# Performance work log

Hardware: AMD Instinct MI355X
Metric: run time of the kernel (lower is better)

Reference implementation:

```python
import jax, jax.numpy as jnp
import numpy as np

N_NODES = 50000
N_EDGES = 200000
IN_DIM = 512
HID = 2000
LAT = 128


def setup_inputs() -> dict:
    key = jax.random.key(0)
    ks = jax.random.split(key, 6)
    x = jax.random.normal(ks[0], (N_NODES, IN_DIM), dtype=jnp.float32)
    edge_index = jax.random.randint(ks[1], (2, N_EDGES), 0, N_NODES, dtype=jnp.int64)
    # glorot-ish scales so ReLU/Sigmoid stay in a sane range
    W1 = jax.random.normal(ks[2], (IN_DIM, HID), dtype=jnp.float32) * (1.0 / np.sqrt(IN_DIM))
    b1 = jnp.zeros((HID,), dtype=jnp.float32)
    W2 = jax.random.normal(ks[3], (HID, LAT), dtype=jnp.float32) * (1.0 / np.sqrt(HID))
    b2 = jnp.zeros((LAT,), dtype=jnp.float32)
    return {"x": x, "edge_index": edge_index, "W1": W1, "b1": b1, "W2": W2, "b2": b2}


def gcn_conv(x, edge_index, W, b):
    """PyG GCNConv: D^-1/2 (A+I) D^-1/2 (X W) + b, unit edge weights."""
    n = x.shape[0]
    loops = jnp.arange(n, dtype=edge_index.dtype)
    row = jnp.concatenate([edge_index[0], loops])  # source nodes
    col = jnp.concatenate([edge_index[1], loops])  # target nodes
    deg = jax.ops.segment_sum(jnp.ones_like(col, dtype=x.dtype), col, num_segments=n)
    dis = jnp.where(deg > 0, jax.lax.rsqrt(deg), 0.0)  # deg^-1/2, inf -> 0
    norm = dis[row] * dis[col]                         # [E+N]
    h = x @ W                                          # transform first: [N, out]
    msg = h[row] * norm[:, None]                       # gather + normalize: [E+N, out]
    out = jax.ops.segment_sum(msg, col, num_segments=n)  # scatter-add
    return out + b


def reference(x, edge_index, W1, b1, W2, b2):
    h = jax.nn.relu(gcn_conv(x, edge_index, W1, b1))
    return jax.nn.sigmoid(gcn_conv(h, edge_index, W2, b2))
```

## Files before the change

### kernel.cpp

```cpp
#include <hip/hip_runtime.h>
#include <hip/hip_fp16.h>

#define NN 50000
#define NE 200000
#define IND 512
#define HIDD 2000
#define LATD 128

#define M_PAD 50176
#define N1_PAD 2048
#define MT1 392
#define NBLK 196

typedef _Float16 f16x8 __attribute__((ext_vector_type(8)));
typedef float f32x4 __attribute__((ext_vector_type(4)));

__device__ __forceinline__ void gload_lds16(const _Float16* g, _Float16* l) {
    __builtin_amdgcn_global_load_lds(
        (const __attribute__((address_space(1))) unsigned int*)g,
        (__attribute__((address_space(3))) unsigned int*)l,
        16, 0, 0);
}

__global__ void k_degree(const int* __restrict__ col, int* __restrict__ deg) {
    int e = blockIdx.x * 256 + threadIdx.x;
    if (e < NE) atomicAdd(&deg[col[e]], 1);
}

__global__ void k_bsum(const int* __restrict__ deg, int* __restrict__ bsum) {
    __shared__ int sm[4];
    int i = blockIdx.x * 256 + threadIdx.x;
    int v = (i < NN) ? deg[i] : 0;
    #pragma unroll
    for (int off = 32; off; off >>= 1) v += __shfl_down(v, off, 64);
    if ((threadIdx.x & 63) == 0) sm[threadIdx.x >> 6] = v;
    __syncthreads();
    if (threadIdx.x == 0) bsum[blockIdx.x] = sm[0] + sm[1] + sm[2] + sm[3];
}

__global__ void k_bscan(int* __restrict__ bsum) {
    __shared__ int sm[256];
    int tid = threadIdx.x;
    int v = (tid < NBLK) ? bsum[tid] : 0;
    sm[tid] = v;
    __syncthreads();
    #pragma unroll
    for (int off = 1; off < 256; off <<= 1) {
        int t = (tid >= off) ? sm[tid - off] : 0;
        __syncthreads();
        sm[tid] += t;
        __syncthreads();
    }
    if (tid < NBLK) bsum[tid] = sm[tid] - v;
}

__global__ void k_scan_final(const int* __restrict__ deg, const int* __restrict__ bsum,
                             int* __restrict__ row_ptr, float* __restrict__ dis) {
    __shared__ int sm[256];
    int b = blockIdx.x, tid = threadIdx.x;
    int i = b * 256 + tid;
    int v = (i < NN) ? deg[i] : 0;
    if (i < NN) dis[i] = rsqrtf((float)v + 1.0f);
    sm[tid] = v;
    __syncthreads();
    #pragma unroll
    for (int off = 1; off < 256; off <<= 1) {
        int t = (tid >= off) ? sm[tid - off] : 0;
        __syncthreads();
        sm[tid] += t;
        __syncthreads();
    }
    if (i < NN) row_ptr[i] = bsum[b] + sm[tid] - v;
    if (i == NN - 1) row_ptr[NN] = bsum[b] + sm[tid];
}

__global__ void k_fill(const int* __restrict__ ei, const int* __restrict__ row_ptr,
                       int* __restrict__ cursor, int* __restrict__ csr_src) {
    int e = blockIdx.x * 256 + threadIdx.x;
    if (e < NE) {
        int r = ei[e], c = ei[NE + e];
        int pos = atomicAdd(&cursor[c], 1);
        csr_src[row_ptr[c] + pos] = r;
    }
}

__global__ void k_transpose_tiled(const float* __restrict__ in,
                                  _Float16* __restrict__ out, int R, int C, int ldo,
                                  int Rpad, int Cpad) {
    __shared__ float sm[32][33];
    int c0 = blockIdx.x * 32, r0 = blockIdx.y * 32;
    int tx = threadIdx.x & 31, ty = threadIdx.x >> 5;
    #pragma unroll
    for (int i = 0; i < 4; ++i) {
        int r = r0 + ty + i * 8, c = c0 + tx;
        sm[ty + i * 8][tx] = (r < R && c < C) ? in[(size_t)r * C + c] : 0.f;
    }
    __syncthreads();
    #pragma unroll
    for (int i = 0; i < 4; ++i) {
        int c = c0 + ty + i * 8, r = r0 + tx;
        if (c < Cpad && r < Rpad) out[(size_t)c * ldo + r] = (_Float16)sm[tx][ty + i * 8];
    }
}

__global__ void k_xcvt(const float* __restrict__ in, _Float16* __restrict__ out, int n8) {
    int i = blockIdx.x * 256 + threadIdx.x;
    if (i < n8) {
        float4 a = ((const float4*)in)[i * 2];
        float4 b = ((const float4*)in)[i * 2 + 1];
        f16x8 o;
        o[0] = (_Float16)a.x; o[1] = (_Float16)a.y; o[2] = (_Float16)a.z; o[3] = (_Float16)a.w;
        o[4] = (_Float16)b.x; o[5] = (_Float16)b.y; o[6] = (_Float16)b.z; o[7] = (_Float16)b.w;
        ((f16x8*)out)[i] = o;
    }
}

__global__ void k_gather_x(const _Float16* __restrict__ xh, const int* __restrict__ row_ptr,
                           const int* __restrict__ csr_src, const float* __restrict__ dis,
                           _Float16* __restrict__ Ah) {
    int dst = blockIdx.x * 4 + (threadIdx.x >> 6);
    if (dst >= NN) return;
    int lane = threadIdx.x & 63;
    float dd = dis[dst];
    const f16x8* vb = (const f16x8*)xh;
    f16x8 sv = vb[(size_t)dst * 64 + lane];
    float acc[8];
    #pragma unroll
    for (int q = 0; q < 8; ++q) acc[q] = dd * (float)sv[q];
    int beg = row_ptr[dst], end = row_ptr[dst + 1];
    for (int c = beg; c < end; c += 64) {
        int n = end - c; if (n > 64) n = 64;
        int li = (lane < n) ? csr_src[c + lane] : 0;
        float lns = (lane < n) ? dis[li] : 0.f;
        for (int j = 0; j < n; j += 4) {
            int j1 = j + 1 < n ? j + 1 : n - 1;
            int j2 = j + 2 < n ? j + 2 : n - 1;
            int j3 = j + 3 < n ? j + 3 : n - 1;
            int s0 = __shfl(li, j),  s1 = __shfl(li, j1);
            int s2 = __shfl(li, j2), s3 = __shfl(li, j3);
            float w0 = __shfl(lns, j);
            float w1 = (j + 1 < n) ? __shfl(lns, j1) : 0.f;
            float w2 = (j + 2 < n) ? __shfl(lns, j2) : 0.f;
            float w3 = (j + 3 < n) ? __shfl(lns, j3) : 0.f;
            f16x8 v0 = vb[(size_t)s0 * 64 + lane];
            f16x8 v1 = vb[(size_t)s1 * 64 + lane];
            f16x8 v2 = vb[(size_t)s2 * 64 + lane];
            f16x8 v3 = vb[(size_t)s3 * 64 + lane];
            #pragma unroll
            for (int q = 0; q < 8; ++q)
                acc[q] += w0 * (float)v0[q] + w1 * (float)v1[q]
                        + w2 * (float)v2[q] + w3 * (float)v3[q];
        }
    }
    f16x8 o;
    #pragma unroll
    for (int q = 0; q < 8; ++q) o[q] = (_Float16)(dd * acc[q]);
    *(f16x8*)(Ah + (size_t)dst * IND + lane * 8) = o;
}

__global__ void k_gather_t(const float* __restrict__ t, const int* __restrict__ row_ptr,
                           const int* __restrict__ csr_src, const float* __restrict__ dis,
                           const float* __restrict__ b2, float* __restrict__ out) {
    int dst = blockIdx.x * 4 + (threadIdx.x >> 6);
    if (dst >= NN) return;
    int lane = threadIdx.x & 63;
    float dd = dis[dst];
    const float2* vb = (const float2*)t;
    float2 td = vb[(size_t)dst * 64 + lane];
    float accx = dd * td.x, accy = dd * td.y;
    int beg = row_ptr[dst], end = row_ptr[dst + 1];
    for (int c = beg; c < end; c += 64) {
        int n = end - c; if (n > 64) n = 64;
        int li = (lane < n) ? csr_src[c + lane] : 0;
        float lns = (lane < n) ? dis[li] : 0.f;
        for (int j = 0; j < n; j += 4) {
            int j1 = j + 1 < n ? j + 1 : n - 1;
            int j2 = j + 2 < n ? j + 2 : n - 1;
            int j3 = j + 3 < n ? j + 3 : n - 1;
            int s0 = __shfl(li, j),  s1 = __shfl(li, j1);
            int s2 = __shfl(li, j2), s3 = __shfl(li, j3);
            float w0 = __shfl(lns, j);
            float w1 = (j + 1 < n) ? __shfl(lns, j1) : 0.f;
            float w2 = (j + 2 < n) ? __shfl(lns, j2) : 0.f;
            float w3 = (j + 3 < n) ? __shfl(lns, j3) : 0.f;
            float2 v0 = vb[(size_t)s0 * 64 + lane];
            float2 v1 = vb[(size_t)s1 * 64 + lane];
            float2 v2 = vb[(size_t)s2 * 64 + lane];
            float2 v3 = vb[(size_t)s3 * 64 + lane];
            accx += w0 * v0.x + w1 * v1.x + w2 * v2.x + w3 * v3.x;
            accy += w0 * v0.y + w1 * v1.y + w2 * v2.y + w3 * v3.y;
        }
    }
    float2 bb = *(const float2*)(b2 + lane * 2);
    float vx = dd * accx + bb.x;
    float vy = dd * accy + bb.y;
    float2 o;
    o.x = 1.0f / (1.0f + __expf(-vx));
    o.y = 1.0f / (1.0f + __expf(-vy));
    *(float2*)(out + (size_t)dst * LATD + lane * 2) = o;
}

__global__ __launch_bounds__(256, 2) void k_gemm1(
    const _Float16* __restrict__ A,
    const _Float16* __restrict__ Bt,
    const float* __restrict__ bias,
    _Float16* __restrict__ Ch,
    int mT0, int slab)
{
    const int b = blockIdx.x;
    const int mT = mT0 + (b & 7) * slab + ((b >> 3) >> 4);
    const int nT = (b >> 3) & 15;
    const int mBase = mT * 128;
    const int nBase = nT * 128;

    __shared__ __align__(16) _Float16 As[2 * 128 * 32];
    __shared__ __align__(16) _Float16 Bs[2 * 128 * 32];

    const int tid = threadIdx.x;
    const int lane = tid & 63;
    const int w = tid >> 6;

    const int srow = w * 32 + (lane >> 2);
    const int scol = (lane & 3) * 8;
    const _Float16* Ag0 = A + (size_t)(mBase + srow) * IND + scol;
    const _Float16* Ag1 = Ag0 + (size_t)16 * IND;
    const _Float16* Bg0 = Bt + (size_t)(nBase + srow) * IND + scol;
    const _Float16* Bg1 = Bg0 + (size_t)16 * IND;

    const int wm = (w >> 1) * 64;
    const int wn = (w & 1) * 64;
    const int lm = lane & 15;
    const int quad = lane >> 4;

    f32x4 acc[4][4];
    #pragma unroll
    for (int i = 0; i < 4; ++i)
        #pragma unroll
        for (int j = 0; j < 4; ++j)
            acc[i][j] = (f32x4){0.f, 0.f, 0.f, 0.f};

    for (int k0 = 0; k0 < IND; k0 += 64) {
        #pragma unroll
        for (int s = 0; s < 2; ++s) {
            gload_lds16(Ag0 + k0 + s * 32, As + s * 4096 + w * 1024);
            gload_lds16(Ag1 + k0 + s * 32, As + s * 4096 + w * 1024 + 512);
            gload_lds16(Bg0 + k0 + s * 32, Bs + s * 4096 + w * 1024);
            gload_lds16(Bg1 + k0 + s * 32, Bs + s * 4096 + w * 1024 + 512);
        }
        __syncthreads();

        #pragma unroll
        for (int s = 0; s < 2; ++s) {
            f16x8 af[4], bfr[4];
            #pragma unroll
            for (int mi = 0; mi < 4; ++mi)
                af[mi] = *(const f16x8*)&As[s * 4096 + (wm + mi * 16 + lm) * 32 + quad * 8];
            #pragma unroll
            for (int ni = 0; ni < 4; ++ni)
                bfr[ni] = *(const f16x8*)&Bs[s * 4096 + (wn + ni * 16 + lm) * 32 + quad * 8];
            #pragma unroll
            for (int mi = 0; mi < 4; ++mi)
                #pragma unroll
                for (int ni = 0; ni < 4; ++ni)
                    acc[mi][ni] = __builtin_amdgcn_mfma_f32_16x16x32_f16(
                        af[mi], bfr[ni], acc[mi][ni], 0, 0, 0);
        }
        __syncthreads();
    }

    #pragma unroll
    for (int mi = 0; mi < 4; ++mi) {
        #pragma unroll
        for (int ni = 0; ni < 4; ++ni) {
            int col = nBase + wn + ni * 16 + lm;
            float bval = (col < HIDD) ? bias[col] : 0.f;
            #pragma unroll
            for (int r = 0; r < 4; ++r) {
                int rowg = mBase + wm + mi * 16 + quad * 4 + r;
                float v = fmaxf(acc[mi][ni][r] + bval, 0.f);
                Ch[(size_t)rowg * N1_PAD + col] = (_Float16)v;
            }
        }
    }
}

__global__ __launch_bounds__(256, 2) void k_gemm2(
    const _Float16* __restrict__ A,
    const _Float16* __restrict__ Bt,
    float* __restrict__ Cf)
{
    __shared__ __align__(16) _Float16 As[2 * 4096];
    __shared__ __align__(16) _Float16 Bs[2 * 8192];

    const int tid = threadIdx.x;
    const int lane = tid & 63;
    const int w = tid >> 6;
    const int mBase = blockIdx.x * 64;

    const int srA = w * 16 + (lane >> 2);
    const int srB = w * 32 + (lane >> 2);
    const int scol = (lane & 3) * 8;
    const _Float16* Ag  = A + (size_t)(mBase + srA) * N1_PAD + scol;
    const _Float16* Bg0 = Bt + (size_t)srB * N1_PAD + scol;
    const _Float16* Bg1 = Bg0 + (size_t)16 * N1_PAD;

    const int wm = (w & 1) * 32;
    const int wn = (w >> 1) * 64;
    const int lm = lane & 15;
    const int quad = lane >> 4;

    f32x4 acc[2][4];
    #pragma unroll
    for (int i = 0; i < 2; ++i)
        #pragma unroll
        for (int j = 0; j < 4; ++j)
            acc[i][j] = (f32x4){0.f, 0.f, 0.f, 0.f};

    auto STAGE = [&](int buf, int k0) {
        #pragma unroll
        for (int s = 0; s < 2; ++s) {
            gload_lds16(Ag + k0 + s * 32, As + buf * 4096 + s * 2048 + w * 512);
            gload_lds16(Bg0 + k0 + s * 32, Bs + buf * 8192 + s * 4096 + w * 1024);
            gload_lds16(Bg1 + k0 + s * 32, Bs + buf * 8192 + s * 4096 + w * 1024 + 512);
        }
    };
    auto COMPUTE = [&](int buf) {
        #pragma unroll
        for (int s = 0; s < 2; ++s) {
            f16x8 af[2], bfr[4];
            #pragma unroll
            for (int mi = 0; mi < 2; ++mi)
                af[mi] = *(const f16x8*)&As[buf * 4096 + s * 2048 + (wm + mi * 16 + lm) * 32 + quad * 8];
            #pragma unroll
            for (int ni = 0; ni < 4; ++ni)
                bfr[ni] = *(const f16x8*)&Bs[buf * 8192 + s * 4096 + (wn + ni * 16 + lm) * 32 + quad * 8];
            #pragma unroll
            for (int mi = 0; mi < 2; ++mi)
                #pragma unroll
                for (int ni = 0; ni < 4; ++ni)
                    acc[mi][ni] = __builtin_amdgcn_mfma_f32_16x16x32_f16(
                        af[mi], bfr[ni], acc[mi][ni], 0, 0, 0);
        }
    };

    STAGE(0, 0);
    __syncthreads();
    #pragma unroll 1
    for (int it = 0; it < 15; ++it) {
        STAGE(1, (2 * it + 1) * 64);
        COMPUTE(0);
        __syncthreads();
        STAGE(0, (2 * it + 2) * 64);
        COMPUTE(1);
        __syncthreads();
    }
    STAGE(1, 31 * 64);
    COMPUTE(0);
    __syncthreads();
    COMPUTE(1);

    #pragma unroll
    for (int mi = 0; mi < 2; ++mi) {
        #pragma unroll
        for (int ni = 0; ni < 4; ++ni) {
            int col = wn + ni * 16 + lm;
            #pragma unroll
            for (int r = 0; r < 4; ++r) {
                int rowg = mBase + wm + mi * 16 + quad * 4 + r;
                Cf[(size_t)rowg * LATD + col] = acc[mi][ni][r];
            }
        }
    }
}

extern "C" void kernel_launch(void* const* d_in, const int* in_sizes, int n_in,
                              void* d_out, int out_size, void* d_ws, size_t ws_size,
                              hipStream_t stream) {
    const float* x  = (const float*)d_in[0];
    const int* ei   = (const int*)d_in[1];
    const float* W1 = (const float*)d_in[2];
    const float* b1 = (const float*)d_in[3];
    const float* W2 = (const float*)d_in[4];
    const float* b2 = (const float*)d_in[5];
    float* out = (float*)d_out;

    char* p = (char*)d_ws;
    auto alloc = [&](size_t bytes) {
        char* q = p; p += (bytes + 255) & ~(size_t)255; return q;
    };
    int* deg        = (int*)alloc((size_t)NN * 4);
    int* bsum       = (int*)alloc((size_t)NBLK * 4);
    int* row_ptr    = (int*)alloc((size_t)(NN + 1) * 4);
    int* cursor     = (int*)alloc((size_t)NN * 4);
    int* csr_src    = (int*)alloc((size_t)NE * 4);
    float* dis      = (float*)alloc((size_t)NN * 4);
    _Float16* W1T   = (_Float16*)alloc((size_t)N1_PAD * IND * 2);
    _Float16* W2T   = (_Float16*)alloc((size_t)LATD * N1_PAD * 2);
    _Float16* xh    = (_Float16*)alloc((size_t)NN * IND * 2);
    _Float16* Ah    = (_Float16*)alloc((size_t)M_PAD * IND * 2);
    _Float16* h     = (_Float16*)alloc((size_t)M_PAD * N1_PAD * 2);
    float* t        = (float*)alloc((size_t)M_PAD * LATD * 4);

    hipMemsetAsync(deg,    0, (size_t)NN * 4, stream);
    hipMemsetAsync(cursor, 0, (size_t)NN * 4, stream);

    k_degree<<<(NE + 255) / 256, 256, 0, stream>>>(ei + NE, deg);
    k_bsum<<<NBLK, 256, 0, stream>>>(deg, bsum);
    k_bscan<<<1, 256, 0, stream>>>(bsum);
    k_scan_final<<<NBLK, 256, 0, stream>>>(deg, bsum, row_ptr, dis);
    k_fill<<<(NE + 255) / 256, 256, 0, stream>>>(ei, row_ptr, cursor, csr_src);

    {
        dim3 gt1(N1_PAD / 32, IND / 32);
        k_transpose_tiled<<<gt1, 256, 0, stream>>>(W1, W1T, IND, HIDD, IND, IND, N1_PAD);
        dim3 gt2(LATD / 32, N1_PAD / 32);
        k_transpose_tiled<<<gt2, 256, 0, stream>>>(W2, W2T, HIDD, LATD, N1_PAD, N1_PAD, LATD);
        k_xcvt<<<(NN * IND / 8 + 255) / 256, 256, 0, stream>>>(x, xh, NN * IND / 8);
    }

    k_gather_x<<<(NN + 3) / 4, 256, 0, stream>>>(xh, row_ptr, csr_src, dis, Ah);

    k_gemm1<<<8 * 12 * 16, 256, 0, stream>>>(Ah, W1T, b1, h, 0,   12);
    k_gemm1<<<8 * 12 * 16, 256, 0, stream>>>(Ah, W1T, b1, h, 96,  12);
    k_gemm1<<<8 * 12 * 16, 256, 0, stream>>>(Ah, W1T, b1, h, 192, 12);
    k_gemm1<<<8 * 13 * 16, 256, 0, stream>>>(Ah, W1T, b1, h, 288, 13);
    k_gemm2<<<M_PAD / 64, 256, 0, stream>>>(h, W2T, t);

    k_gather_t<<<(NN + 3) / 4, 256, 0, stream>>>(t, row_ptr, csr_src, dis, b2, out);
}
```

Baseline: 502.4 us.

## Fuse both GEMMs into one kernel keeping hidden activations in LDS

Replaces the four GEMM1 launches and the separate GEMM2 with a single kernel. Each block computes 128-column chunks of the ReLU hidden layer for 64 rows, stores them in shared memory, and immediately multiplies them by the matching slice of W2. This removes the write and re-read of the 50176x2048 fp16 hidden matrix. In exchange, each block streams its A tile from global memory again for every chunk and reads W2 fragments directly from global. The GEMM1 tile shrinks to 64x128, and the loop is not double-buffered.

```diff
diff --git a/kernel.cpp b/kernel.cpp
--- a/kernel.cpp
+++ b/kernel.cpp
@@ -9,7 +9,6 @@
 
 #define M_PAD 50176
 #define N1_PAD 2048
-#define MT1 392
 #define NBLK 196
 
 typedef _Float16 f16x8 __attribute__((ext_vector_type(8)));
@@ -200,164 +199,112 @@
     *(float2*)(out + (size_t)dst * LATD + lane * 2) = o;
 }
 
-__global__ __launch_bounds__(256, 2) void k_gemm1(
+__global__ __launch_bounds__(256, 3) void k_fused(
     const _Float16* __restrict__ A,
-    const _Float16* __restrict__ Bt,
-    const float* __restrict__ bias,
-    _Float16* __restrict__ Ch,
-    int mT0, int slab)
-{
-    const int b = blockIdx.x;
-    const int mT = mT0 + (b & 7) * slab + ((b >> 3) >> 4);
-    const int nT = (b >> 3) & 15;
-    const int mBase = mT * 128;
-    const int nBase = nT * 128;
-
-    __shared__ __align__(16) _Float16 As[2 * 128 * 32];
-    __shared__ __align__(16) _Float16 Bs[2 * 128 * 32];
-
-    const int tid = threadIdx.x;
-    const int lane = tid & 63;
-    const int w = tid >> 6;
-
-    const int srow = w * 32 + (lane >> 2);
-    const int scol = (lane & 3) * 8;
-    const _Float16* Ag0 = A + (size_t)(mBase + srow) * IND + scol;
-    const _Float16* Ag1 = Ag0 + (size_t)16 * IND;
-    const _Float16* Bg0 = Bt + (size_t)(nBase + srow) * IND + scol;
-    const _Float16* Bg1 = Bg0 + (size_t)16 * IND;
-
-    const int wm = (w >> 1) * 64;
-    const int wn = (w & 1) * 64;
-    const int lm = lane & 15;
-    const int quad = lane >> 4;
-
-    f32x4 acc[4][4];
-    #pragma unroll
-    for (int i = 0; i < 4; ++i)
-        #pragma unroll
-        for (int j = 0; j < 4; ++j)
-            acc[i][j] = (f32x4){0.f, 0.f, 0.f, 0.f};
-
-    for (int k0 = 0; k0 < IND; k0 += 64) {
-        #pragma unroll
-        for (int s = 0; s < 2; ++s) {
-            gload_lds16(Ag0 + k0 + s * 32, As + s * 4096 + w * 1024);
-            gload_lds16(Ag1 + k0 + s * 32, As + s * 4096 + w * 1024 + 512);
-            gload_lds16(Bg0 + k0 + s * 32, Bs + s * 4096 + w * 1024);
-            gload_lds16(Bg1 + k0 + s * 32, Bs + s * 4096 + w * 1024 + 512);
-        }
-        __syncthreads();
-
-        #pragma unroll
-        for (int s = 0; s < 2; ++s) {
-            f16x8 af[4], bfr[4];
-            #pragma unroll
-            for (int mi = 0; mi < 4; ++mi)
-                af[mi] = *(const f16x8*)&As[s * 4096 + (wm + mi * 16 + lm) * 32 + quad * 8];
-            #pragma unroll
-            for (int ni = 0; ni < 4; ++ni)
-                bfr[ni] = *(const f16x8*)&Bs[s * 4096 + (wn + ni * 16 + lm) * 32 + quad * 8];
-            #pragma unroll
-            for (int mi = 0; mi < 4; ++mi)
-                #pragma unroll
-                for (int ni = 0; ni < 4; ++ni)
-                    acc[mi][ni] = __builtin_amdgcn_mfma_f32_16x16x32_f16(
-                        af[mi], bfr[ni], acc[mi][ni], 0, 0, 0);
-        }
-        __syncthreads();
-    }
-
-    #pragma unroll
-    for (int mi = 0; mi < 4; ++mi) {
-        #pragma unroll
-        for (int ni = 0; ni < 4; ++ni) {
-            int col = nBase + wn + ni * 16 + lm;
-            float bval = (col < HIDD) ? bias[col] : 0.f;
-            #pragma unroll
-            for (int r = 0; r < 4; ++r) {
-                int rowg = mBase + wm + mi * 16 + quad * 4 + r;
-                float v = fmaxf(acc[mi][ni][r] + bval, 0.f);
-                Ch[(size_t)rowg * N1_PAD + col] = (_Float16)v;
-            }
-        }
-    }
-}
-
-__global__ __launch_bounds__(256, 2) void k_gemm2(
-    const _Float16* __restrict__ A,
-    const _Float16* __restrict__ Bt,
+    const _Float16* __restrict__ B1,
+    const float* __restrict__ b1,
+    const _Float16* __restrict__ B2,
     float* __restrict__ Cf)
 {
-    __shared__ __align__(16) _Float16 As[2 * 4096];
-    __shared__ __align__(16) _Float16 Bs[2 * 8192];
+    __shared__ __align__(16) _Float16 As[2 * 64 * 32];
+    __shared__ __align__(16) _Float16 Bs[2 * 128 * 32];
+    __shared__ __align__(16) _Float16 hs[64 * 136];
 
     const int tid = threadIdx.x;
     const int lane = tid & 63;
     const int w = tid >> 6;
     const int mBase = blockIdx.x * 64;
 
-    const int srA = w * 16 + (lane >> 2);
-    const int srB = w * 32 + (lane >> 2);
+    const int srowA = w * 16 + (lane >> 2);
+    const int srowB = w * 32 + (lane >> 2);
     const int scol = (lane & 3) * 8;
-    const _Float16* Ag  = A + (size_t)(mBase + srA) * N1_PAD + scol;
-    const _Float16* Bg0 = Bt + (size_t)srB * N1_PAD + scol;
-    const _Float16* Bg1 = Bg0 + (size_t)16 * N1_PAD;
+    const _Float16* Ag = A + (size_t)(mBase + srowA) * IND + scol;
 
     const int wm = (w & 1) * 32;
     const int wn = (w >> 1) * 64;
     const int lm = lane & 15;
     const int quad = lane >> 4;
 
-    f32x4 acc[2][4];
+    f32x4 acc2[2][4];
     #pragma unroll
     for (int i = 0; i < 2; ++i)
         #pragma unroll
         for (int j = 0; j < 4; ++j)
-            acc[i][j] = (f32x4){0.f, 0.f, 0.f, 0.f};
-
-    auto STAGE = [&](int buf, int k0) {
-        #pragma unroll
-        for (int s = 0; s < 2; ++s) {
-            gload_lds16(Ag + k0 + s * 32, As + buf * 4096 + s * 2048 + w * 512);
-            gload_lds16(Bg0 + k0 + s * 32, Bs + buf * 8192 + s * 4096 + w * 1024);
-            gload_lds16(Bg1 + k0 + s * 32, Bs + buf * 8192 + s * 4096 + w * 1024 + 512);
-        }
-    };
-    auto COMPUTE = [&](int buf) {
-        #pragma unroll
-        for (int s = 0; s < 2; ++s) {
-            f16x8 af[2], bfr[4];
+            acc2[i][j] = (f32x4){0.f, 0.f, 0.f, 0.f};
+
+    #pragma unroll 1
+    for (int nc = 0; nc < 16; ++nc) {
+        f32x4 acc1[2][4];
+        #pragma unroll
+        for (int i = 0; i < 2; ++i)
+            #pragma unroll
+            for (int j = 0; j < 4; ++j)
+                acc1[i][j] = (f32x4){0.f, 0.f, 0.f, 0.f};
+
+        const _Float16* Bg0 = B1 + (size_t)(nc * 128 + srowB) * IND + scol;
+        const _Float16* Bg1 = Bg0 + (size_t)16 * IND;
+
+        for (int k0 = 0; k0 < IND; k0 += 64) {
+            #pragma unroll
+            for (int s = 0; s < 2; ++s) {
+                gload_lds16(Ag + k0 + s * 32, As + s * 2048 + w * 512);
+                gload_lds16(Bg0 + k0 + s * 32, Bs + s * 4096 + w * 1024);
+                gload_lds16(Bg1 + k0 + s * 32, Bs + s * 4096 + w * 1024 + 512);
+            }
+            __syncthreads();
+            #pragma unroll
+            for (int s = 0; s < 2; ++s) {
+                f16x8 af[2], bfr[4];
+                #pragma unroll
+                for (int mi = 0; mi < 2; ++mi)
+                    af[mi] = *(const f16x8*)&As[s * 2048 + (wm + mi * 16 + lm) * 32 + quad * 8];
+                #pragma unroll
+                for (int ni = 0; ni < 4; ++ni)
+                    bfr[ni] = *(const f16x8*)&Bs[s * 4096 + (wn + ni * 16 + lm) * 32 + quad * 8];
+                #pragma unroll
+                for (int mi = 0; mi < 2; ++mi)
+                    #pragma unroll
+                    for (int ni = 0; ni < 4; ++ni)
+                        acc1[mi][ni] = __builtin_amdgcn_mfma_f32_16x16x32_f16(
+                            af[mi], bfr[ni], acc1[mi][ni], 0, 0, 0);
+            }
+            __syncthreads();
+        }
+
+        #pragma unroll
+        for (int mi = 0; mi < 2; ++mi) {
+            #pragma unroll
+            for (int ni = 0; ni < 4; ++ni) {
+                int col = wn + ni * 16 + lm;
+                int gcol = nc * 128 + col;
+                float bval = (gcol < HIDD) ? b1[gcol] : 0.f;
+                #pragma unroll
+                for (int r = 0; r < 4; ++r) {
+                    int row = wm + mi * 16 + quad * 4 + r;
+                    hs[row * 136 + col] = (_Float16)fmaxf(acc1[mi][ni][r] + bval, 0.f);
+                }
+            }
+        }
+        __syncthreads();
+
+        #pragma unroll
+        for (int ks = 0; ks < 4; ++ks) {
+            f16x8 a2[2], b2f[4];
             #pragma unroll
             for (int mi = 0; mi < 2; ++mi)
-                af[mi] = *(const f16x8*)&As[buf * 4096 + s * 2048 + (wm + mi * 16 + lm) * 32 + quad * 8];
+                a2[mi] = *(const f16x8*)&hs[(wm + mi * 16 + lm) * 136 + ks * 32 + quad * 8];
             #pragma unroll
             for (int ni = 0; ni < 4; ++ni)
-                bfr[ni] = *(const f16x8*)&Bs[buf * 8192 + s * 4096 + (wn + ni * 16 + lm) * 32 + quad * 8];
+                b2f[ni] = *(const f16x8*)(B2 + (size_t)(wn + ni * 16 + lm) * N1_PAD
+                                          + nc * 128 + ks * 32 + quad * 8);
             #pragma unroll
             for (int mi = 0; mi < 2; ++mi)
                 #pragma unroll
                 for (int ni = 0; ni < 4; ++ni)
-                    acc[mi][ni] = __builtin_amdgcn_mfma_f32_16x16x32_f16(
-                        af[mi], bfr[ni], acc[mi][ni], 0, 0, 0);
-        }
-    };
-
-    STAGE(0, 0);
-    __syncthreads();
-    #pragma unroll 1
-    for (int it = 0; it < 15; ++it) {
-        STAGE(1, (2 * it + 1) * 64);
-        COMPUTE(0);
-        __syncthreads();
-        STAGE(0, (2 * it + 2) * 64);
-        COMPUTE(1);
-        __syncthreads();
-    }
-    STAGE(1, 31 * 64);
-    COMPUTE(0);
-    __syncthreads();
-    COMPUTE(1);
+                    acc2[mi][ni] = __builtin_amdgcn_mfma_f32_16x16x32_f16(
+                        a2[mi], b2f[ni], acc2[mi][ni], 0, 0, 0);
+        }
+    }
 
     #pragma unroll
     for (int mi = 0; mi < 2; ++mi) {
@@ -367,7 +314,7 @@
             #pragma unroll
             for (int r = 0; r < 4; ++r) {
                 int rowg = mBase + wm + mi * 16 + quad * 4 + r;
-                Cf[(size_t)rowg * LATD + col] = acc[mi][ni][r];
+                Cf[(size_t)rowg * LATD + col] = acc2[mi][ni][r];
             }
         }
     }
@@ -398,7 +345,6 @@
     _Float16* W2T   = (_Float16*)alloc((size_t)LATD * N1_PAD * 2);
     _Float16* xh    = (_Float16*)alloc((size_t)NN * IND * 2);
     _Float16* Ah    = (_Float16*)alloc((size_t)M_PAD * IND * 2);
-    _Float16* h     = (_Float16*)alloc((size_t)M_PAD * N1_PAD * 2);
     float* t        = (float*)alloc((size_t)M_PAD * LATD * 4);
 
     hipMemsetAsync(deg,    0, (size_t)NN * 4, stream);
@@ -420,11 +366,7 @@
 
     k_gather_x<<<(NN + 3) / 4, 256, 0, stream>>>(xh, row_ptr, csr_src, dis, Ah);
 
-    k_gemm1<<<8 * 12 * 16, 256, 0, stream>>>(Ah, W1T, b1, h, 0,   12);
-    k_gemm1<<<8 * 12 * 16, 256, 0, stream>>>(Ah, W1T, b1, h, 96,  12);
-    k_gemm1<<<8 * 12 * 16, 256, 0, stream>>>(Ah, W1T, b1, h, 192, 12);
-    k_gemm1<<<8 * 13 * 16, 256, 0, stream>>>(Ah, W1T, b1, h, 288, 13);
-    k_gemm2<<<M_PAD / 64, 256, 0, stream>>>(h, W2T, t);
+    k_fused<<<M_PAD / 64, 256, 0, stream>>>(Ah, W1T, b1, W2T, t);
 
     k_gather_t<<<(NN + 3) / 4, 256, 0, stream>>>(t, row_ptr, csr_src, dis, b2, out);
 }
```

Result: slower. 641.0 us (+27.6%).

## Enlarge gemm2 tile to 128 rows, store t in fp16, drop double buffering

Applied to the files above, without the earlier changes.

The second GEMM now works on 128x128 tiles with 4x4 MFMA fragments per wave, launched as 392 blocks in an interleaved order, and uses a single LDS buffer with a sync after loading instead of the previous double-buffered pipeline. The intermediate t is written and gathered in fp16 rather than fp32, halving the traffic of the final gather and of the GEMM output. The larger tile improves reuse of the loaded data, but dropping the overlap exposes load latency. The fp16 intermediate also loses a little precision.

```diff
diff --git a/kernel.cpp b/kernel.cpp
--- a/kernel.cpp
+++ b/kernel.cpp
@@ -9,10 +9,10 @@
 
 #define M_PAD 50176
 #define N1_PAD 2048
-#define MT1 392
 #define NBLK 196
 
 typedef _Float16 f16x8 __attribute__((ext_vector_type(8)));
+typedef _Float16 f16x2 __attribute__((ext_vector_type(2)));
 typedef float f32x4 __attribute__((ext_vector_type(4)));
 
 __device__ __forceinline__ void gload_lds16(const _Float16* g, _Float16* l) {
@@ -158,16 +158,16 @@
     *(f16x8*)(Ah + (size_t)dst * IND + lane * 8) = o;
 }
 
-__global__ void k_gather_t(const float* __restrict__ t, const int* __restrict__ row_ptr,
+__global__ void k_gather_t(const _Float16* __restrict__ t, const int* __restrict__ row_ptr,
                            const int* __restrict__ csr_src, const float* __restrict__ dis,
                            const float* __restrict__ b2, float* __restrict__ out) {
     int dst = blockIdx.x * 4 + (threadIdx.x >> 6);
     if (dst >= NN) return;
     int lane = threadIdx.x & 63;
     float dd = dis[dst];
-    const float2* vb = (const float2*)t;
-    float2 td = vb[(size_t)dst * 64 + lane];
-    float accx = dd * td.x, accy = dd * td.y;
+    const f16x2* vb = (const f16x2*)t;
+    f16x2 td = vb[(size_t)dst * 64 + lane];
+    float accx = dd * (float)td[0], accy = dd * (float)td[1];
     int beg = row_ptr[dst], end = row_ptr[dst + 1];
     for (int c = beg; c < end; c += 64) {
         int n = end - c; if (n > 64) n = 64;
@@ -183,12 +183,14 @@
             float w1 = (j + 1 < n) ? __shfl(lns, j1) : 0.f;
             float w2 = (j + 2 < n) ? __shfl(lns, j2) : 0.f;
             float w3 = (j + 3 < n) ? __shfl(lns, j3) : 0.f;
-            float2 v0 = vb[(size_t)s0 * 64 + lane];
-            float2 v1 = vb[(size_t)s1 * 64 + lane];
-            float2 v2 = vb[(size_t)s2 * 64 + lane];
-            float2 v3 = vb[(size_t)s3 * 64 + lane];
-            accx += w0 * v0.x + w1 * v1.x + w2 * v2.x + w3 * v3.x;
-            accy += w0 * v0.y + w1 * v1.y + w2 * v2.y + w3 * v3.y;
+            f16x2 v0 = vb[(size_t)s0 * 64 + lane];
+            f16x2 v1 = vb[(size_t)s1 * 64 + lane];
+            f16x2 v2 = vb[(size_t)s2 * 64 + lane];
+            f16x2 v3 = vb[(size_t)s3 * 64 + lane];
+            accx += w0 * (float)v0[0] + w1 * (float)v1[0]
+                  + w2 * (float)v2[0] + w3 * (float)v3[0];
+            accy += w0 * (float)v0[1] + w1 * (float)v1[1]
+                  + w2 * (float)v2[1] + w3 * (float)v3[1];
         }
     }
     float2 bb = *(const float2*)(b2 + lane * 2);
@@ -287,87 +289,76 @@
 __global__ __launch_bounds__(256, 2) void k_gemm2(
     const _Float16* __restrict__ A,
     const _Float16* __restrict__ Bt,
-    float* __restrict__ Cf)
+    _Float16* __restrict__ Cf)
 {
-    __shared__ __align__(16) _Float16 As[2 * 4096];
-    __shared__ __align__(16) _Float16 Bs[2 * 8192];
+    const int b = blockIdx.x;
+    const int mT = (b & 7) * 49 + (b >> 3);
+    const int mBase = mT * 128;
+
+    __shared__ __align__(16) _Float16 As[2 * 128 * 32];
+    __shared__ __align__(16) _Float16 Bs[2 * 128 * 32];
 
     const int tid = threadIdx.x;
     const int lane = tid & 63;
     const int w = tid >> 6;
-    const int mBase = blockIdx.x * 64;
-
-    const int srA = w * 16 + (lane >> 2);
-    const int srB = w * 32 + (lane >> 2);
+
+    const int srow = w * 32 + (lane >> 2);
     const int scol = (lane & 3) * 8;
-    const _Float16* Ag  = A + (size_t)(mBase + srA) * N1_PAD + scol;
-    const _Float16* Bg0 = Bt + (size_t)srB * N1_PAD + scol;
+    const _Float16* Ag0 = A + (size_t)(mBase + srow) * N1_PAD + scol;
+    const _Float16* Ag1 = Ag0 + (size_t)16 * N1_PAD;
+    const _Float16* Bg0 = Bt + (size_t)srow * N1_PAD + scol;
     const _Float16* Bg1 = Bg0 + (size_t)16 * N1_PAD;
 
-    const int wm = (w & 1) * 32;
-    const int wn = (w >> 1) * 64;
+    const int wm = (w >> 1) * 64;
+    const int wn = (w & 1) * 64;
     const int lm = lane & 15;
     const int quad = lane >> 4;
 
-    f32x4 acc[2][4];
-    #pragma unroll
-    for (int i = 0; i < 2; ++i)
+    f32x4 acc[4][4];
+    #pragma unroll
+    for (int i = 0; i < 4; ++i)
         #pragma unroll
         for (int j = 0; j < 4; ++j)
             acc[i][j] = (f32x4){0.f, 0.f, 0.f, 0.f};
 
-    auto STAGE = [&](int buf, int k0) {
+    for (int k0 = 0; k0 < N1_PAD; k0 += 64) {
         #pragma unroll
         for (int s = 0; s < 2; ++s) {
-            gload_lds16(Ag + k0 + s * 32, As + buf * 4096 + s * 2048 + w * 512);
-            gload_lds16(Bg0 + k0 + s * 32, Bs + buf * 8192 + s * 4096 + w * 1024);
-            gload_lds16(Bg1 + k0 + s * 32, Bs + buf * 8192 + s * 4096 + w * 1024 + 512);
-        }
-    };
-    auto COMPUTE = [&](int buf) {
+            gload_lds16(Ag0 + k0 + s * 32, As + s * 4096 + w * 1024);
+            gload_lds16(Ag1 + k0 + s * 32, As + s * 4096 + w * 1024 + 512);
+            gload_lds16(Bg0 + k0 + s * 32, Bs + s * 4096 + w * 1024);
+            gload_lds16(Bg1 + k0 + s * 32, Bs + s * 4096 + w * 1024 + 512);
+        }
+        __syncthreads();
+
         #pragma unroll
         for (int s = 0; s < 2; ++s) {
-            f16x8 af[2], bfr[4];
-            #pragma unroll
-            for (int mi = 0; mi < 2; ++mi)
-                af[mi] = *(const f16x8*)&As[buf * 4096 + s * 2048 + (wm + mi * 16 + lm) * 32 + quad * 8];
+            f16x8 af[4], bfr[4];
+            #pragma unroll
+            for (int mi = 0; mi < 4; ++mi)
+                af[mi] = *(const f16x8*)&As[s * 4096 + (wm + mi * 16 + lm) * 32 + quad * 8];
             #pragma unroll
             for (int ni = 0; ni < 4; ++ni)
-                bfr[ni] = *(const f16x8*)&Bs[buf * 8192 + s * 4096 + (wn + ni * 16 + lm) * 32 + quad * 8];
-            #pragma unroll
-            for (int mi = 0; mi < 2; ++mi)
+                bfr[ni] = *(const f16x8*)&Bs[s * 4096 + (wn + ni * 16 + lm) * 32 + quad * 8];
+            #pragma unroll
+            for (int mi = 0; mi < 4; ++mi)
                 #pragma unroll
                 for (int ni = 0; ni < 4; ++ni)
                     acc[mi][ni] = __builtin_amdgcn_mfma_f32_16x16x32_f16(
                         af[mi], bfr[ni], acc[mi][ni], 0, 0, 0);
         }
-    };
-
-    STAGE(0, 0);
-    __syncthreads();
-    #pragma unroll 1
-    for (int it = 0; it < 15; ++it) {
-        STAGE(1, (2 * it + 1) * 64);
-        COMPUTE(0);
-        __syncthreads();
-        STAGE(0, (2 * it + 2) * 64);
-        COMPUTE(1);
-        __syncthreads();
-    }
-    STAGE(1, 31 * 64);
-    COMPUTE(0);
-    __syncthreads();
-    COMPUTE(1);
-
-    #pragma unroll
-    for (int mi = 0; mi < 2; ++mi) {
+        __syncthreads();
+    }
+
+    #pragma unroll
+    for (int mi = 0; mi < 4; ++mi) {
         #pragma unroll
         for (int ni = 0; ni < 4; ++ni) {
             int col = wn + ni * 16 + lm;
             #pragma unroll
             for (int r = 0; r < 4; ++r) {
                 int rowg = mBase + wm + mi * 16 + quad * 4 + r;
-                Cf[(size_t)rowg * LATD + col] = acc[mi][ni][r];
+                Cf[(size_t)rowg * LATD + col] = (_Float16)acc[mi][ni][r];
             }
         }
     }
@@ -399,7 +390,7 @@
     _Float16* xh    = (_Float16*)alloc((size_t)NN * IND * 2);
     _Float16* Ah    = (_Float16*)alloc((size_t)M_PAD * IND * 2);
     _Float16* h     = (_Float16*)alloc((size_t)M_PAD * N1_PAD * 2);
-    float* t        = (float*)alloc((size_t)M_PAD * LATD * 4);
+    _Float16* t     = (_Float16*)alloc((size_t)M_PAD * LATD * 2);
 
     hipMemsetAsync(deg,    0, (size_t)NN * 4, stream);
     hipMemsetAsync(cursor, 0, (size_t)NN * 4, stream);
@@ -424,7 +415,8 @@
     k_gemm1<<<8 * 12 * 16, 256, 0, stream>>>(Ah, W1T, b1, h, 96,  12);
     k_gemm1<<<8 * 12 * 16, 256, 0, stream>>>(Ah, W1T, b1, h, 192, 12);
     k_gemm1<<<8 * 13 * 16, 256, 0, stream>>>(Ah, W1T, b1, h, 288, 13);
-    k_gemm2<<<M_PAD / 64, 256, 0, stream>>>(h, W2T, t);
+
+    k_gemm2<<<392, 256, 0, stream>>>(h, W2T, t);
 
     k_gather_t<<<(NN + 3) / 4, 256, 0, stream>>>(t, row_ptr, csr_src, dis, b2, out);
 }
```

Result: no change. 500.6 us (-0.3%).
